# Optimization experiments

Measured on AMD Instinct MI355X. Metric: run time of the kernel, lower is better.

## Reference

```python
import jax, jax.numpy as jnp
from jax import lax
import numpy as np

B, C, H, W = 8, 256, 25, 512
KS = 9
EPS = 1e-5


def setup_inputs() -> dict:
    key = jax.random.key(0)
    ks = jax.random.split(key, 5)
    return {
        "p2_c": jax.random.normal(ks[0], (B, C, H, W), jnp.float32),
        # conv_u_d weight [O,I,9,1]; small scale keeps the 25-step recurrence stable
        "w_msg": jax.random.normal(ks[1], (C, C, KS, 1), jnp.float32) * 0.02,
        "gamma1": jnp.ones((C,), jnp.float32),
        "beta1": jnp.zeros((C,), jnp.float32),
        # conv_up2 adapted to 256->256 (original 64->64 is inconsistent with the data flow)
        "w_up2": jax.random.normal(ks[2], (C, C, 3, 3), jnp.float32) * 0.02,
        "w_conv1": jax.random.normal(ks[3], (1, C, 1, 1), jnp.float32) * 0.05,  # 256->1 1x1
        "w_conv2": jax.random.normal(ks[4], (1, H, 1, 1), jnp.float32) * 0.05,  # 25->1 1x1
    }


def _c_scnn(x, M):
    # x: [B,C,H,W]. Row recurrence: out[0]=x[0]; out[i]=x[i]+relu(M @ out[i-1]).
    # The (9,1) conv on a height-1 slice with pad 4 uses only the center kernel
    # row, i.e. a pure channel-mixing matmul M=[O,I]. Final output is reversed
    # along H exactly as in the original (out[::-1]).
    xs = jnp.moveaxis(x, 2, 0)  # [H,B,C,W]

    def step(prev, xi):
        cur = xi + jax.nn.relu(jnp.einsum('oi,biw->bow', M, prev))
        return cur, cur

    _, rest = lax.scan(step, xs[0], xs[1:])
    outs = jnp.concatenate([xs[:1], rest], axis=0)[::-1]  # reversed rows
    return jnp.moveaxis(outs, 0, 2)  # [B,C,H,W]


def _bn(x, gamma, beta):
    # BatchNorm2d in training mode: per-channel batch stats (biased variance)
    mean = jnp.mean(x, axis=(0, 2, 3), keepdims=True)
    var = jnp.var(x, axis=(0, 2, 3), keepdims=True)
    g = gamma.reshape(1, -1, 1, 1)
    b = beta.reshape(1, -1, 1, 1)
    return g * (x - mean) * lax.rsqrt(var + EPS) + b


def _up_w(x):
    # F.interpolate(size=(H, 2W), mode='bilinear', align_corners=True):
    # height is identity; width is doubled with align_corners mapping.
    w = x.shape[-1]
    wn = 2 * w
    pos = jnp.arange(wn, dtype=x.dtype) * ((w - 1) / (wn - 1))
    i0 = jnp.floor(pos).astype(jnp.int32)
    i1 = jnp.minimum(i0 + 1, w - 1)
    frac = (pos - i0.astype(x.dtype))
    return x[..., i0] * (1.0 - frac) + x[..., i1] * frac


def reference(p2_c, w_msg, gamma1, beta1, w_up2, w_conv1, w_conv2):
    M = w_msg[:, :, KS // 2, 0]  # effective 1x1 channel-mix matrix [O,I]
    x = jax.nn.relu(_bn(_c_scnn(p2_c, M), gamma1, beta1))
    x = jax.nn.relu(_bn(_c_scnn(x, M), gamma1, beta1))
    x = _up_w(x)                                        # [B,256,25,2W]
    x = lax.conv_general_dilated(
        x, w_up2, window_strides=(1, 1), padding=((1, 1), (1, 1)),
        dimension_numbers=('NCHW', 'OIHW', 'NCHW'))     # 3x3 conv
    x = _up_w(x)                                        # [B,256,25,4W]
    x = jnp.einsum('oc,bchw->bohw', w_conv1[:, :, 0, 0], x)  # [B,1,25,4W]
    x = _up_w(x)                                        # [B,1,25,8W]
    x = jnp.transpose(x, (0, 2, 1, 3))                  # [B,25,1,8W]
    x = jnp.einsum('oh,bhcw->bocw', w_conv2[:, :, 0, 0], x)  # [B,1,1,8W]
    return jax.nn.sigmoid(x)
```

## Files before the change

### kernel.cpp

```cpp
#include <hip/hip_runtime.h>
#include <math.h>


#define XBF_OFF    0
#define YBF_OFF    13107200
#define MBF_OFF    26214400
#define COEF1_OFF  26247168
#define COEF2_OFF  26247680
#define WH_OFF     26248192
#define T_OFF      26267392
#define ST1_OFF    26279680
#define ST2_OFF    26280192
#define R_OFF      26280704
#define ZERO_FLOATS 13312

typedef __attribute__((ext_vector_type(8))) short bf16x8;
typedef __attribute__((ext_vector_type(4))) float f32x4;

__device__ __forceinline__ ushort f2bf(float f) {
    uint32_t b = __float_as_uint(f);
    b += 0x7fffu + ((b >> 16) & 1u);
    return (ushort)(b >> 16);
}
__device__ __forceinline__ float bf2f(ushort u) {
    return __uint_as_float((uint32_t)u << 16);
}

__global__ __launch_bounds__(256) void prep_mbf(const float* __restrict__ wmsg,
                                                ushort* __restrict__ Mbf)
{
    int idx = blockIdx.x * 256 + threadIdx.x;
    Mbf[idx] = f2bf(wmsg[(size_t)idx * 9 + 4]);
}

__global__ __launch_bounds__(256) void prep_wh(const float* __restrict__ wup2,
                                               const float* __restrict__ w1,
                                               const float* __restrict__ w2,
                                               float* __restrict__ wh)
{
    const int c  = blockIdx.x / 3;
    const int kw = blockIdx.x % 3;
    const int o  = threadIdx.x;
    const float w1o = w1[o];
    __shared__ float red[3][256];
    red[0][o] = w1o * wup2[(size_t)((o * 256 + c) * 3 + 0) * 3 + kw];
    red[1][o] = w1o * wup2[(size_t)((o * 256 + c) * 3 + 1) * 3 + kw];
    red[2][o] = w1o * wup2[(size_t)((o * 256 + c) * 3 + 2) * 3 + kw];
    __syncthreads();
    for (int st = 128; st > 0; st >>= 1) {
        if (o < st) {
            red[0][o] += red[0][o + st];
            red[1][o] += red[1][o + st];
            red[2][o] += red[2][o + st];
        }
        __syncthreads();
    }
    if (o < 25) {
        float s = 0.f;
        #pragma unroll
        for (int kh = 0; kh < 3; ++kh) {
            int m = o - kh + 1;
            if (m >= 0 && m < 25) s = fmaf(w2[m], red[kh][0], s);
        }
        wh[(c * 25 + o) * 3 + kw] = s;
    }
}

template <bool INBF>
__global__ __launch_bounds__(512, 2) void scnn_mfma(const void* __restrict__ xin_,
                                                    const ushort* __restrict__ Mbf,
                                                    ushort* __restrict__ outb,
                                                    const float* __restrict__ coef,
                                                    float* __restrict__ stats)
{
    __shared__ ulong2 lds_[1024];
    char* lds = (char*)lds_;
    const float*  xf = (const float*)xin_;
    const ushort* xh = (const ushort*)xin_;

    const int tid   = threadIdx.x;
    const int lane  = tid & 63;
    const int wid   = tid >> 6;
    const int row16 = lane & 15;
    const int g     = lane >> 4;
    const int b     = blockIdx.x >> 5;
    const int w0    = (blockIdx.x & 31) << 4;
    const int to0   = wid * 2;

    const int lofs = (lane * 16) ^ (((lane >> 4) & 1) << 5);
    int woff[2];
    #pragma unroll
    for (int tt = 0; tt < 2; ++tt) {
        int inner = (tt * 2 + (g >> 1)) * 256 + row16 * 16 + (g & 1) * 8;
        woff[tt] = wid * 1024 + (inner ^ (((inner >> 8) & 1) << 5));
    }

    bf16x8 afrag[2][8];
    #pragma unroll
    for (int tt = 0; tt < 2; ++tt) {
        const ushort* mrow = Mbf + (size_t)((to0 + tt) * 16 + row16) * 256 + g * 8;
        #pragma unroll
        for (int kk = 0; kk < 8; ++kk)
            afrag[tt][kk] = *reinterpret_cast<const bf16x8*>(mrow + kk * 32);
    }

    const bool hasbn = (coef != nullptr);
    float ca[2][4], cb[2][4];
    if (hasbn) {
        #pragma unroll
        for (int tt = 0; tt < 2; ++tt)
            #pragma unroll
            for (int r = 0; r < 4; ++r) {
                int o = (to0 + tt) * 16 + g * 4 + r;
                ca[tt][r] = coef[o];
                cb[tt][r] = coef[256 + o];
            }
    }

    size_t base[2][4];
    #pragma unroll
    for (int tt = 0; tt < 2; ++tt)
        #pragma unroll
        for (int r = 0; r < 4; ++r) {
            int o = (to0 + tt) * 16 + g * 4 + r;
            base[tt][r] = (size_t)(b * 256 + o) * 25 * 512 + w0 + row16;
        }

    uint xv[2][4], xn[2][4];
    #define LDX(t, dst)                                                        \
        { _Pragma("unroll") for (int tt = 0; tt < 2; ++tt)                     \
          _Pragma("unroll") for (int r = 0; r < 4; ++r) {                      \
              size_t a = base[tt][r] + (size_t)(t) * 512;                      \
              dst[tt][r] = INBF ? (uint)xh[a] : __float_as_uint(xf[a]);        \
          } }

    LDX(0, xv);
    LDX(1, xn);

    float s1[2][4] = {{0,0,0,0},{0,0,0,0}};
    float sq[2][4] = {{0,0,0,0},{0,0,0,0}};

    int p = 0;
    for (int t = 0; t < 25; ++t) {
        uint x2[2][4] = {{0,0,0,0},{0,0,0,0}};
        if (t < 23) LDX(t + 2, x2);

        f32x4 acc[2] = {{0.f,0.f,0.f,0.f},{0.f,0.f,0.f,0.f}};
        if (t > 0) {
            const char* pb = lds + p * 8192 + lofs;
            #pragma unroll
            for (int kk = 0; kk < 8; ++kk) {
                bf16x8 bfr = *reinterpret_cast<const bf16x8*>(pb + kk * 1024);
                acc[0] = __builtin_amdgcn_mfma_f32_16x16x32_bf16(afrag[0][kk], bfr, acc[0], 0, 0, 0);
                acc[1] = __builtin_amdgcn_mfma_f32_16x16x32_bf16(afrag[1][kk], bfr, acc[1], 0, 0, 0);
            }
        }

        char* wb = lds + (p ^ 1) * 8192;
        #pragma unroll
        for (int tt = 0; tt < 2; ++tt) {
            ushort us[4];
            #pragma unroll
            for (int r = 0; r < 4; ++r) {
                float x = INBF ? bf2f((ushort)xv[tt][r]) : __uint_as_float(xv[tt][r]);
                if (hasbn) x = fmaxf(fmaf(ca[tt][r], x, cb[tt][r]), 0.0f);
                float cv = x + fmaxf(acc[tt][r], 0.0f);
                us[r] = f2bf(cv);
                outb[base[tt][r] + (size_t)(24 - t) * 512] = us[r];
                s1[tt][r] += cv;
                sq[tt][r] = fmaf(cv, cv, sq[tt][r]);
            }
            *reinterpret_cast<ushort4*>(wb + woff[tt]) =
                make_ushort4(us[0], us[1], us[2], us[3]);
        }

        asm volatile("s_waitcnt lgkmcnt(0)" ::: "memory");
        __builtin_amdgcn_s_barrier();
        __builtin_amdgcn_sched_barrier(0);

        p ^= 1;
        #pragma unroll
        for (int tt = 0; tt < 2; ++tt)
            #pragma unroll
            for (int r = 0; r < 4; ++r) { xv[tt][r] = xn[tt][r]; xn[tt][r] = x2[tt][r]; }
    }

    #pragma unroll
    for (int tt = 0; tt < 2; ++tt)
        #pragma unroll
        for (int r = 0; r < 4; ++r) {
            float a = s1[tt][r], q = sq[tt][r];
            #pragma unroll
            for (int m = 8; m >= 1; m >>= 1) {
                a += __shfl_xor(a, m, 64);
                q += __shfl_xor(q, m, 64);
            }
            if (row16 == 0) {
                int o = (to0 + tt) * 16 + g * 4 + r;
                atomicAdd(&stats[o], a);
                atomicAdd(&stats[256 + o], q);
            }
        }
}

__global__ __launch_bounds__(256) void coef_kernel(const float* __restrict__ stats,
                                                   const float* __restrict__ gamma,
                                                   const float* __restrict__ beta,
                                                   float* __restrict__ coef)
{
    int c = threadIdx.x;
    float mean = stats[c] * (1.0f / 102400.0f);
    float var  = stats[256 + c] * (1.0f / 102400.0f) - mean * mean;
    float a = gamma[c] * rsqrtf(var + 1e-5f);
    coef[c] = a;
    coef[256 + c] = beta[c] - mean * a;
}

__global__ __launch_bounds__(256) void conv_reduce(const ushort* __restrict__ Y,
                                                   const float* __restrict__ coef2,
                                                   const float* __restrict__ wh,
                                                   float* __restrict__ T)
{
    const int v2 = threadIdx.x;
    const int b  = blockIdx.x >> 5;
    const int c0 = (blockIdx.x & 31) << 3;

    __shared__ float whL[8][25][3];
    for (int i = threadIdx.x; i < 600; i += 256) {
        int ci = i / 75, rem = i % 75;
        whL[ci][rem / 3][rem % 3] = wh[(c0 + ci) * 75 + rem];
    }
    __syncthreads();

    float a0[2] = {0,0}, a1[2] = {0,0}, a2[2] = {0,0};
    for (int ci = 0; ci < 8; ++ci) {
        int c = c0 + ci;
        float sa = coef2[c], bo = coef2[256 + c];
        const uint* rowb = (const uint*)(Y + (size_t)(b * 256 + c) * 12800) + v2;
        #pragma unroll 5
        for (int hh = 0; hh < 25; ++hh) {
            uint yy = rowb[hh * 256];
            float z0 = fmaxf(fmaf(sa, bf2f((ushort)(yy & 0xffffu)), bo), 0.f);
            float z1 = fmaxf(fmaf(sa, bf2f((ushort)(yy >> 16)),     bo), 0.f);
            float wc0 = whL[ci][hh][0], wc1 = whL[ci][hh][1], wc2 = whL[ci][hh][2];
            a0[0] = fmaf(wc0, z0, a0[0]); a0[1] = fmaf(wc0, z1, a0[1]);
            a1[0] = fmaf(wc1, z0, a1[0]); a1[1] = fmaf(wc1, z1, a1[1]);
            a2[0] = fmaf(wc2, z0, a2[0]); a2[1] = fmaf(wc2, z1, a2[1]);
        }
    }
    const int vb = 2 * v2;
    atomicAdd(&T[(0 * 8 + b) * 512 + vb],     a0[0]);
    atomicAdd(&T[(0 * 8 + b) * 512 + vb + 1], a0[1]);
    atomicAdd(&T[(1 * 8 + b) * 512 + vb],     a1[0]);
    atomicAdd(&T[(1 * 8 + b) * 512 + vb + 1], a1[1]);
    atomicAdd(&T[(2 * 8 + b) * 512 + vb],     a2[0]);
    atomicAdd(&T[(2 * 8 + b) * 512 + vb + 1], a2[1]);
}

__global__ __launch_bounds__(256) void combine_r(const float* __restrict__ T,
                                                 float* __restrict__ r)
{
    int idx = blockIdx.x * 256 + threadIdx.x;
    int b = idx >> 10, w = idx & 1023;
    const float scale = (float)(511.0 / 1023.0);
    float acc = 0.f;
    #pragma unroll
    for (int kw = 0; kw < 3; ++kw) {
        int u = w + kw - 1;
        if (u >= 0 && u < 1024) {
            float pos = (float)u * scale;
            int i0 = (int)pos;
            float f = pos - (float)i0;
            int i1 = min(i0 + 1, 511);
            const float* Tk = T + (size_t)(kw * 8 + b) * 512;
            float lo = Tk[i0];
            acc += fmaf(Tk[i1] - lo, f, lo);
        }
    }
    r[idx] = acc;
}

__global__ __launch_bounds__(256) void final_kernel(const float* __restrict__ r,
                                                    float* __restrict__ out)
{
    int idx = blockIdx.x * 256 + threadIdx.x;
    int b = idx >> 12, w4 = idx & 4095;
    const float s3 = (float)(2047.0 / 4095.0);
    const float s2 = (float)(1023.0 / 2047.0);
    const float* rb = r + b * 1024;

    float pos3 = (float)w4 * s3;
    int j0 = (int)pos3;
    float f3 = pos3 - (float)j0;
    int j1 = min(j0 + 1, 2047);

    float v[2];
    int jj[2] = {j0, j1};
    #pragma unroll
    for (int k = 0; k < 2; ++k) {
        float p = (float)jj[k] * s2;
        int i = (int)p;
        float f = p - (float)i;
        int i2 = min(i + 1, 1023);
        float lo = rb[i];
        v[k] = fmaf(rb[i2] - lo, f, lo);
    }
    float z = fmaf(v[1] - v[0], f3, v[0]);
    out[idx] = 1.0f / (1.0f + expf(-z));
}

extern "C" void kernel_launch(void* const* d_in, const int* in_sizes, int n_in,
                              void* d_out, int out_size, void* d_ws, size_t ws_size,
                              hipStream_t stream)
{
    const float* p2c   = (const float*)d_in[0];
    const float* wmsg  = (const float*)d_in[1];
    const float* gamma = (const float*)d_in[2];
    const float* beta  = (const float*)d_in[3];
    const float* wup2  = (const float*)d_in[4];
    const float* wc1   = (const float*)d_in[5];
    const float* wc2   = (const float*)d_in[6];
    float* out = (float*)d_out;
    float* ws  = (float*)d_ws;

    ushort* Xbf   = (ushort*)(ws + XBF_OFF);
    ushort* Ybf   = (ushort*)(ws + YBF_OFF);
    ushort* Mbf   = (ushort*)(ws + MBF_OFF);
    float*  coef1 = ws + COEF1_OFF;
    float*  coef2 = ws + COEF2_OFF;
    float*  wh    = ws + WH_OFF;
    float*  T     = ws + T_OFF;
    float*  st1   = ws + ST1_OFF;
    float*  st2   = ws + ST2_OFF;
    float*  r     = ws + R_OFF;

    hipMemsetAsync(T, 0, ZERO_FLOATS * sizeof(float), stream);

    prep_mbf<<<256, 256, 0, stream>>>(wmsg, Mbf);
    prep_wh<<<768, 256, 0, stream>>>(wup2, wc1, wc2, wh);

    scnn_mfma<false><<<256, 512, 0, stream>>>(p2c, Mbf, Xbf, nullptr, st1);
    coef_kernel<<<1, 256, 0, stream>>>(st1, gamma, beta, coef1);

    scnn_mfma<true><<<256, 512, 0, stream>>>(Xbf, Mbf, Ybf, coef1, st2);
    coef_kernel<<<1, 256, 0, stream>>>(st2, gamma, beta, coef2);

    conv_reduce<<<256, 256, 0, stream>>>(Ybf, coef2, wh, T);
    combine_r<<<32, 256, 0, stream>>>(T, r);

    final_kernel<<<128, 256, 0, stream>>>(r, out);
}
```

Measured before the change: 176.8 us.

## Preload all 25 rows of inputs into registers and fully unroll the recurrence

After: 616.4 us. 249% more time.

```diff
diff --git a/kernel.cpp b/kernel.cpp
--- a/kernel.cpp
+++ b/kernel.cpp
@@ -117,37 +117,37 @@
             }
     }
 
-    size_t base[2][4];
+    uint ofs[2][4];
     #pragma unroll
     for (int tt = 0; tt < 2; ++tt)
         #pragma unroll
         for (int r = 0; r < 4; ++r) {
             int o = (to0 + tt) * 16 + g * 4 + r;
-            base[tt][r] = (size_t)(b * 256 + o) * 25 * 512 + w0 + row16;
-        }
-
-    uint xv[2][4], xn[2][4];
-    #define LDX(t, dst)                                                        \
-        { _Pragma("unroll") for (int tt = 0; tt < 2; ++tt)                     \
-          _Pragma("unroll") for (int r = 0; r < 4; ++r) {                      \
-              size_t a = base[tt][r] + (size_t)(t) * 512;                      \
-              dst[tt][r] = INBF ? (uint)xh[a] : __float_as_uint(xf[a]);        \
-          } }
-
-    LDX(0, xv);
-    LDX(1, xn);
+            ofs[tt][r] = (uint)((b * 256 + o) * 12800 + w0 + row16);
+        }
+
+    uint xreg[100];
+    #pragma unroll
+    for (int t = 0; t < 25; ++t)
+        #pragma unroll
+        for (int tt = 0; tt < 2; ++tt)
+            #pragma unroll
+            for (int rq = 0; rq < 2; ++rq) {
+                uint a0 = ofs[tt][2 * rq]     + (uint)t * 512u;
+                uint a1 = ofs[tt][2 * rq + 1] + (uint)t * 512u;
+                ushort lo = INBF ? xh[a0] : f2bf(xf[a0]);
+                ushort hi = INBF ? xh[a1] : f2bf(xf[a1]);
+                xreg[t * 4 + tt * 2 + rq] = (uint)lo | ((uint)hi << 16);
+            }
 
     float s1[2][4] = {{0,0,0,0},{0,0,0,0}};
     float sq[2][4] = {{0,0,0,0},{0,0,0,0}};
 
-    int p = 0;
+    #pragma unroll
     for (int t = 0; t < 25; ++t) {
-        uint x2[2][4] = {{0,0,0,0},{0,0,0,0}};
-        if (t < 23) LDX(t + 2, x2);
-
         f32x4 acc[2] = {{0.f,0.f,0.f,0.f},{0.f,0.f,0.f,0.f}};
         if (t > 0) {
-            const char* pb = lds + p * 8192 + lofs;
+            const char* pb = lds + (t & 1) * 8192 + lofs;
             #pragma unroll
             for (int kk = 0; kk < 8; ++kk) {
                 bf16x8 bfr = *reinterpret_cast<const bf16x8*>(pb + kk * 1024);
@@ -156,17 +156,17 @@
             }
         }
 
-        char* wb = lds + (p ^ 1) * 8192;
+        char* wb = lds + ((t & 1) ^ 1) * 8192;
         #pragma unroll
         for (int tt = 0; tt < 2; ++tt) {
             ushort us[4];
             #pragma unroll
             for (int r = 0; r < 4; ++r) {
-                float x = INBF ? bf2f((ushort)xv[tt][r]) : __uint_as_float(xv[tt][r]);
+                float x = bf2f((ushort)(xreg[t * 4 + tt * 2 + (r >> 1)] >> ((r & 1) * 16)));
                 if (hasbn) x = fmaxf(fmaf(ca[tt][r], x, cb[tt][r]), 0.0f);
                 float cv = x + fmaxf(acc[tt][r], 0.0f);
                 us[r] = f2bf(cv);
-                outb[base[tt][r] + (size_t)(24 - t) * 512] = us[r];
+                outb[ofs[tt][r] + (uint)(24 - t) * 512u] = us[r];
                 s1[tt][r] += cv;
                 sq[tt][r] = fmaf(cv, cv, sq[tt][r]);
             }
@@ -174,15 +174,11 @@
                 make_ushort4(us[0], us[1], us[2], us[3]);
         }
 
-        asm volatile("s_waitcnt lgkmcnt(0)" ::: "memory");
-        __builtin_amdgcn_s_barrier();
-        __builtin_amdgcn_sched_barrier(0);
-
-        p ^= 1;
-        #pragma unroll
-        for (int tt = 0; tt < 2; ++tt)
-            #pragma unroll
-            for (int r = 0; r < 4; ++r) { xv[tt][r] = xn[tt][r]; xn[tt][r] = x2[tt][r]; }
+        if (t < 24) {
+            asm volatile("s_waitcnt lgkmcnt(0)" ::: "memory");
+            __builtin_amdgcn_s_barrier();
+            __builtin_amdgcn_sched_barrier(0);
+        }
     }
 
     #pragma unroll
```
